# Performance work log

Measured on AMD Instinct MI355X. Metric: run time of the kernel, lower is better.

Reference implementation:

```python
import jax, jax.numpy as jnp
import numpy as np

N_NODES = 50000
N_EDGES = 800000
D_FEAT = 64
UNITS = 64


def setup_inputs() -> dict:
    key = jax.random.key(0)
    k1, k2, k3, k4, k5 = jax.random.split(key, 5)
    embeddings = jax.random.normal(k1, (N_NODES, D_FEAT), dtype=jnp.float32)
    edge_src = jax.random.randint(k2, (N_EDGES,), 0, N_NODES, dtype=jnp.int32)
    edge_dst = jax.random.randint(k3, (N_EDGES,), 0, N_NODES, dtype=jnp.int32)
    # normalized-adjacency-like positive weights
    edge_w = jax.random.uniform(k4, (N_EDGES,), dtype=jnp.float32)
    # keras 'truncated_normal' initializer default stddev=0.05 (approx w/ normal)
    kernel = jax.random.normal(k5, (D_FEAT, UNITS), dtype=jnp.float32) * 0.05
    return {"embeddings": embeddings, "edge_src": edge_src,
            "edge_dst": edge_dst, "edge_w": edge_w, "kernel": kernel}


def reference(embeddings, edge_src, edge_dst, edge_w, kernel):
    # SpMM: agg[i] = sum_{e: dst(e)=i} w_e * embeddings[src(e)]
    msgs = embeddings[edge_src] * edge_w[:, None]            # [E, D]
    agg = jax.ops.segment_sum(msgs, edge_dst,
                              num_segments=embeddings.shape[0])  # [N, D]
    # dense GEMM + relu (use_bias=False)
    return jax.nn.relu(agg @ kernel)                          # [N, units]
```

## Files before the change

kernel.cpp:

```cpp
#include <hip/hip_runtime.h>
#include <hip/hip_bf16.h>

#define D       64
#define CH      4096
#define BKT     32
#define PASS    1024
#define NCOL    16
#define COLMASK 15
#define SCAP    128
#define SCAPSH  7

__global__ __launch_bounds__(256) void front(
    const float* __restrict__ emb,
    const float* __restrict__ W,
    __hip_bfloat16* __restrict__ Zb,
    const int*   __restrict__ src,
    const int*   __restrict__ dst,
    const float* __restrict__ w,
    int*         __restrict__ gcnt,
    int2*        __restrict__ csr,
    int N, int E, int NB, int NC)
{
    __shared__ int2 rec[CH];
    __shared__ int  lcnt[1568];
    __shared__ int  sh[256];

    const int t = threadIdx.x;

    if ((int)blockIdx.x < NC) {
        const int c     = blockIdx.x;
        const int color = c & COLMASK;
        const int e0    = c * CH;
        const int cnt   = min(CH, E - e0);

        for (int b = t; b < NB; b += 256) lcnt[b] = 0;
        __syncthreads();

        int2 myrec[16]; int mypos[16];
        const int4*   s4p = reinterpret_cast<const int4*>(src + e0);
        const int4*   d4p = reinterpret_cast<const int4*>(dst + e0);
        const float4* w4p = reinterpret_cast<const float4*>(w + e0);
#pragma unroll
        for (int i = 0; i < 4; ++i) {
            int g = i * 256 + t;
            if (g * 4 < cnt) {
                int4   s4 = s4p[g];
                int4   d4 = d4p[g];
                float4 w4 = w4p[g];
                int b0 = d4.x >> 5, b1 = d4.y >> 5, b2 = d4.z >> 5, b3 = d4.w >> 5;
                myrec[4*i+0] = make_int2(s4.x | ((d4.x & 31) << 16) | (b0 << 21), __float_as_int(w4.x));
                myrec[4*i+1] = make_int2(s4.y | ((d4.y & 31) << 16) | (b1 << 21), __float_as_int(w4.y));
                myrec[4*i+2] = make_int2(s4.z | ((d4.z & 31) << 16) | (b2 << 21), __float_as_int(w4.z));
                myrec[4*i+3] = make_int2(s4.w | ((d4.w & 31) << 16) | (b3 << 21), __float_as_int(w4.w));
                mypos[4*i+0] = atomicAdd(&lcnt[b0], 1);
                mypos[4*i+1] = atomicAdd(&lcnt[b1], 1);
                mypos[4*i+2] = atomicAdd(&lcnt[b2], 1);
                mypos[4*i+3] = atomicAdd(&lcnt[b3], 1);
            } else {
#pragma unroll
                for (int k = 0; k < 4; ++k) mypos[4*i+k] = -1;
            }
        }
        __syncthreads();

        int hv[7], ps[7], gbase[7];
        const int hbase = t * 7;
#pragma unroll
        for (int k = 0; k < 7; ++k) {
            int b = hbase + k;
            hv[k] = (b < NB) ? lcnt[b] : 0;
        }
#pragma unroll
        for (int k = 0; k < 7; ++k)
            gbase[k] = (hv[k] > 0)
                ? atomicAdd(&gcnt[color * NB + hbase + k], hv[k]) : 0;

        int s = 0;
#pragma unroll
        for (int k = 0; k < 7; ++k) { ps[k] = s; s += hv[k]; }
        sh[t] = s;
        __syncthreads();
        for (int off = 1; off < 256; off <<= 1) {
            int x = (t >= off) ? sh[t - off] : 0;
            __syncthreads();
            sh[t] += x;
            __syncthreads();
        }
        const int hexcl = sh[t] - s;
        __syncthreads();
#pragma unroll
        for (int k = 0; k < 7; ++k) {
            int b = hbase + k;
            if (b < NB) lcnt[b] = hexcl + ps[k];
        }
        __syncthreads();

#pragma unroll
        for (int k = 0; k < 16; ++k) {
            if (mypos[k] >= 0)
                rec[lcnt[(unsigned)myrec[k].x >> 21] + mypos[k]] = myrec[k];
        }
        __syncthreads();

#pragma unroll
        for (int k = 0; k < 7; ++k) {
            int b = hbase + k;
            if (b < NB)
                lcnt[b] = ((color * NB + b) << SCAPSH) + gbase[k] - (hexcl + ps[k]);
        }
        __syncthreads();

        for (int j = t; j < cnt; j += 256) {
            int2 rj = rec[j];
            csr[j + lcnt[(unsigned)rj.x >> 21]] = rj;
        }
        return;
    }

    float* At = (float*)rec;
    const int row0 = ((int)blockIdx.x - NC) * 64;
    const int lane = t & 63;
    const int wave = t >> 6;

    float wcol[D];
#pragma unroll
    for (int k = 0; k < D; ++k) wcol[k] = W[k * D + lane];

    for (int i = t; i < 1024; i += 256) {
        int r = i >> 4, gr = row0 + r;
        float4 v = (gr < N)
            ? reinterpret_cast<const float4*>(emb)[(size_t)gr * 16 + (i & 15)]
            : float4{0.f, 0.f, 0.f, 0.f};
        reinterpret_cast<float4*>(At)[i] = v;
    }
    __syncthreads();

    for (int rr = 0; rr < 16; ++rr) {
        int r = wave * 16 + rr, gr = row0 + r;
        if (gr >= N) break;
        const float4* arow = reinterpret_cast<const float4*>(At + r * D);
        float acc = 0.f;
#pragma unroll
        for (int k4 = 0; k4 < 16; ++k4) {
            float4 a = arow[k4];
            acc = fmaf(a.x, wcol[4 * k4 + 0], acc);
            acc = fmaf(a.y, wcol[4 * k4 + 1], acc);
            acc = fmaf(a.z, wcol[4 * k4 + 2], acc);
            acc = fmaf(a.w, wcol[4 * k4 + 3], acc);
        }
        Zb[(size_t)gr * D + lane] = __float2bfloat16(acc);
    }
}

__global__ __launch_bounds__(256) void aggregate(
    const __hip_bfloat16* __restrict__ Zb,
    const int2* __restrict__ csr,
    const int*  __restrict__ gcnt,
    float*      __restrict__ out,
    int N, int NB)
{
    __shared__ int2 srec[PASS];
    __shared__ int  hist[BKT];
    __shared__ int  nbase[BKT + 1];
    __shared__ int  cpre[NCOL + 1];

    const int t = threadIdx.x;
    const int b = blockIdx.x;

    if (t == 0) {
        int s = 0;
#pragma unroll
        for (int k = 0; k < NCOL; ++k) { cpre[k] = s; s += gcnt[k * NB + b]; }
        cpre[NCOL] = s;
    }
    __syncthreads();
    const int T = cpre[NCOL];

    const int wv = t >> 6, lane = t & 63, slot = lane >> 3, q = lane & 7;
    const int4* Zq = reinterpret_cast<const int4*>(Zb);

    float4 alo[8], ahi[8];
#pragma unroll
    for (int r = 0; r < 8; ++r) { alo[r] = float4{0,0,0,0}; ahi[r] = float4{0,0,0,0}; }

#define FMA8(LO, HI, WW, ZZ)                                                     \
    do {                                                                         \
        (LO).x = fmaf((WW), __uint_as_float((unsigned)(ZZ).x << 16),        (LO).x); \
        (LO).y = fmaf((WW), __uint_as_float((unsigned)(ZZ).x & 0xFFFF0000u),(LO).y); \
        (LO).z = fmaf((WW), __uint_as_float((unsigned)(ZZ).y << 16),        (LO).z); \
        (LO).w = fmaf((WW), __uint_as_float((unsigned)(ZZ).y & 0xFFFF0000u),(LO).w); \
        (HI).x = fmaf((WW), __uint_as_float((unsigned)(ZZ).z << 16),        (HI).x); \
        (HI).y = fmaf((WW), __uint_as_float((unsigned)(ZZ).z & 0xFFFF0000u),(HI).y); \
        (HI).z = fmaf((WW), __uint_as_float((unsigned)(ZZ).w << 16),        (HI).z); \
        (HI).w = fmaf((WW), __uint_as_float((unsigned)(ZZ).w & 0xFFFF0000u),(HI).w); \
    } while (0)

    for (int cur = 0; cur < T; cur += PASS) {
        const int cnt = min(PASS, T - cur);
        if (t < BKT) hist[t] = 0;
        __syncthreads();

        int2 myrec[4]; int mypos[4];
#pragma unroll
        for (int k = 0; k < 4; ++k) {
            int j = k * 256 + t;
            if (j < cnt) {
                int vj = cur + j;
                int kk = 0;
#pragma unroll
                for (int m = 1; m < NCOL; ++m) kk += (vj >= cpre[m]);
                int2 r2 = csr[((kk * NB + b) << SCAPSH) + (vj - cpre[kk])];
                myrec[k] = r2;
                mypos[k] = atomicAdd(&hist[(r2.x >> 16) & (BKT - 1)], 1);
            } else mypos[k] = -1;
        }
        __syncthreads();

        if (t < BKT) {
            int v = hist[t], x = v;
            for (int off = 1; off < BKT; off <<= 1) {
                int y = __shfl_up(x, off, 64);
                if (t >= off) x += y;
            }
            nbase[t] = x - v;
            if (t == BKT - 1) nbase[BKT] = x;
        }
        __syncthreads();

#pragma unroll
        for (int k = 0; k < 4; ++k) {
            if (mypos[k] >= 0)
                srec[nbase[(myrec[k].x >> 16) & (BKT - 1)] + mypos[k]] = myrec[k];
        }
        __syncthreads();

        for (int r = 0; r < 8; ++r) {
            const int nl = wv * 8 + r;
            const int jb = nbase[nl] + slot;
            const int je = nbase[nl + 1];
            const int j1 = jb + 8, j2 = jb + 16;
            int2 e0 = make_int2(0, 0), e1 = make_int2(0, 0), e2 = make_int2(0, 0);
            if (jb < je) e0 = srec[jb];
            if (j1 < je) e1 = srec[j1];
            if (j2 < je) e2 = srec[j2];
            int4 z0 = make_int4(0,0,0,0), z1 = make_int4(0,0,0,0), z2 = make_int4(0,0,0,0);
            if (jb < je) z0 = Zq[(size_t)(e0.x & 0xFFFF) * 8 + q];
            if (j1 < je) z1 = Zq[(size_t)(e1.x & 0xFFFF) * 8 + q];
            if (j2 < je) z2 = Zq[(size_t)(e2.x & 0xFFFF) * 8 + q];
            FMA8(alo[r], ahi[r], __int_as_float(e0.y), z0);
            FMA8(alo[r], ahi[r], __int_as_float(e1.y), z1);
            FMA8(alo[r], ahi[r], __int_as_float(e2.y), z2);
            for (int j = j2 + 8; j < je; j += 8) {
                int2 e = srec[j];
                int4 zz = Zq[(size_t)(e.x & 0xFFFF) * 8 + q];
                FMA8(alo[r], ahi[r], __int_as_float(e.y), zz);
            }
        }
        __syncthreads();
    }

    const int node0 = b * BKT + wv * 8;
#pragma unroll
    for (int r = 0; r < 8; ++r) {
        float4 lo = alo[r], hi = ahi[r];
#pragma unroll
        for (int off = 32; off >= 8; off >>= 1) {
            lo.x += __shfl_down(lo.x, off, 64);
            lo.y += __shfl_down(lo.y, off, 64);
            lo.z += __shfl_down(lo.z, off, 64);
            lo.w += __shfl_down(lo.w, off, 64);
            hi.x += __shfl_down(hi.x, off, 64);
            hi.y += __shfl_down(hi.y, off, 64);
            hi.z += __shfl_down(hi.z, off, 64);
            hi.w += __shfl_down(hi.w, off, 64);
        }
        int node = node0 + r;
        if (lane < 8 && node < N) {
            float4 o0, o1;
            o0.x = fmaxf(lo.x, 0.f); o0.y = fmaxf(lo.y, 0.f);
            o0.z = fmaxf(lo.z, 0.f); o0.w = fmaxf(lo.w, 0.f);
            o1.x = fmaxf(hi.x, 0.f); o1.y = fmaxf(hi.y, 0.f);
            o1.z = fmaxf(hi.z, 0.f); o1.w = fmaxf(hi.w, 0.f);
            float4* orow = reinterpret_cast<float4*>(out) + (size_t)node * 16 + lane * 2;
            orow[0] = o0;
            orow[1] = o1;
        }
    }
#undef FMA8
}

extern "C" void kernel_launch(void* const* d_in, const int* in_sizes, int n_in,
                              void* d_out, int out_size, void* d_ws, size_t ws_size,
                              hipStream_t stream)
{
    const float* emb  = (const float*)d_in[0];
    const int*   esrc = (const int*)  d_in[1];
    const int*   edst = (const int*)  d_in[2];
    const float* ew   = (const float*)d_in[3];
    const float* W    = (const float*)d_in[4];
    float*       out  = (float*)d_out;

    const int N = in_sizes[0] / D;
    const int E = in_sizes[1];

    const int NB        = (N + BKT - 1) / BKT;
    const int NC        = (E + CH - 1) / CH;
    const int gemmTiles = (N + 63) / 64;

    char* p = (char*)d_ws;
    __hip_bfloat16* Zb = (__hip_bfloat16*)p;  p += (size_t)N * D * 2;
    int*  gcnt = (int*)p;                     p += (size_t)NCOL * ((NB + 3) & ~3) * 4;
    int2* csr  = (int2*)p;

    hipMemsetAsync(gcnt, 0, (size_t)NCOL * NB * sizeof(int), stream);

    front<<<NC + gemmTiles, 256, 0, stream>>>(
        emb, W, Zb, esrc, edst, ew, gcnt, csr, N, E, NB, NC);

    aggregate<<<NB, 256, 0, stream>>>(
        Zb, csr, gcnt, out, N, NB);
}
```

Measured before the change: 127.6 us.

## Interleave two nodes' gathers, make GEMM blocks persistent, parallelize color prefix

```diff
diff --git a/kernel.cpp b/kernel.cpp
--- a/kernel.cpp
+++ b/kernel.cpp
@@ -19,7 +19,7 @@
     const float* __restrict__ w,
     int*         __restrict__ gcnt,
     int2*        __restrict__ csr,
-    int N, int E, int NB, int NC)
+    int N, int E, int NB, int NC, int gemmTiles, int gemmBlocks)
 {
     __shared__ int2 rec[CH];
     __shared__ int  lcnt[1568];
@@ -118,7 +118,6 @@
     }
 
     float* At = (float*)rec;
-    const int row0 = ((int)blockIdx.x - NC) * 64;
     const int lane = t & 63;
     const int wave = t >> 6;
 
@@ -126,29 +125,34 @@
 #pragma unroll
     for (int k = 0; k < D; ++k) wcol[k] = W[k * D + lane];
 
-    for (int i = t; i < 1024; i += 256) {
-        int r = i >> 4, gr = row0 + r;
-        float4 v = (gr < N)
-            ? reinterpret_cast<const float4*>(emb)[(size_t)gr * 16 + (i & 15)]
-            : float4{0.f, 0.f, 0.f, 0.f};
-        reinterpret_cast<float4*>(At)[i] = v;
-    }
-    __syncthreads();
-
-    for (int rr = 0; rr < 16; ++rr) {
-        int r = wave * 16 + rr, gr = row0 + r;
-        if (gr >= N) break;
-        const float4* arow = reinterpret_cast<const float4*>(At + r * D);
-        float acc = 0.f;
-#pragma unroll
-        for (int k4 = 0; k4 < 16; ++k4) {
-            float4 a = arow[k4];
-            acc = fmaf(a.x, wcol[4 * k4 + 0], acc);
-            acc = fmaf(a.y, wcol[4 * k4 + 1], acc);
-            acc = fmaf(a.z, wcol[4 * k4 + 2], acc);
-            acc = fmaf(a.w, wcol[4 * k4 + 3], acc);
-        }
-        Zb[(size_t)gr * D + lane] = __float2bfloat16(acc);
+    for (int tile = (int)blockIdx.x - NC; tile < gemmTiles; tile += gemmBlocks) {
+        const int row0 = tile * 64;
+
+        for (int i = t; i < 1024; i += 256) {
+            int r = i >> 4, gr = row0 + r;
+            float4 v = (gr < N)
+                ? reinterpret_cast<const float4*>(emb)[(size_t)gr * 16 + (i & 15)]
+                : float4{0.f, 0.f, 0.f, 0.f};
+            reinterpret_cast<float4*>(At)[i] = v;
+        }
+        __syncthreads();
+
+        for (int rr = 0; rr < 16; ++rr) {
+            int r = wave * 16 + rr, gr = row0 + r;
+            if (gr >= N) break;
+            const float4* arow = reinterpret_cast<const float4*>(At + r * D);
+            float acc = 0.f;
+#pragma unroll
+            for (int k4 = 0; k4 < 16; ++k4) {
+                float4 a = arow[k4];
+                acc = fmaf(a.x, wcol[4 * k4 + 0], acc);
+                acc = fmaf(a.y, wcol[4 * k4 + 1], acc);
+                acc = fmaf(a.z, wcol[4 * k4 + 2], acc);
+                acc = fmaf(a.w, wcol[4 * k4 + 3], acc);
+            }
+            Zb[(size_t)gr * D + lane] = __float2bfloat16(acc);
+        }
+        __syncthreads();
     }
 }
 
@@ -167,21 +171,22 @@
     const int t = threadIdx.x;
     const int b = blockIdx.x;
 
-    if (t == 0) {
-        int s = 0;
-#pragma unroll
-        for (int k = 0; k < NCOL; ++k) { cpre[k] = s; s += gcnt[k * NB + b]; }
-        cpre[NCOL] = s;
+    if (t < NCOL) {
+        int v = gcnt[t * NB + b];
+        int x = v;
+#pragma unroll
+        for (int off = 1; off < NCOL; off <<= 1) {
+            int y = __shfl_up(x, off, 64);
+            if (t >= off) x += y;
+        }
+        cpre[t] = x - v;
+        if (t == NCOL - 1) cpre[NCOL] = x;
     }
     __syncthreads();
     const int T = cpre[NCOL];
 
     const int wv = t >> 6, lane = t & 63, slot = lane >> 3, q = lane & 7;
     const int4* Zq = reinterpret_cast<const int4*>(Zb);
-
-    float4 alo[8], ahi[8];
-#pragma unroll
-    for (int r = 0; r < 8; ++r) { alo[r] = float4{0,0,0,0}; ahi[r] = float4{0,0,0,0}; }
 
 #define FMA8(LO, HI, WW, ZZ)                                                     \
     do {                                                                         \
@@ -195,6 +200,10 @@
         (HI).w = fmaf((WW), __uint_as_float((unsigned)(ZZ).w & 0xFFFF0000u),(HI).w); \
     } while (0)
 
+    float4 accLo[8], accHi[8];
+#pragma unroll
+    for (int r = 0; r < 8; ++r) { accLo[r] = float4{0,0,0,0}; accHi[r] = float4{0,0,0,0}; }
+
     for (int cur = 0; cur < T; cur += PASS) {
         const int cnt = min(PASS, T - cur);
         if (t < BKT) hist[t] = 0;
@@ -234,26 +243,47 @@
         }
         __syncthreads();
 
-        for (int r = 0; r < 8; ++r) {
-            const int nl = wv * 8 + r;
-            const int jb = nbase[nl] + slot;
-            const int je = nbase[nl + 1];
-            const int j1 = jb + 8, j2 = jb + 16;
-            int2 e0 = make_int2(0, 0), e1 = make_int2(0, 0), e2 = make_int2(0, 0);
-            if (jb < je) e0 = srec[jb];
-            if (j1 < je) e1 = srec[j1];
-            if (j2 < je) e2 = srec[j2];
-            int4 z0 = make_int4(0,0,0,0), z1 = make_int4(0,0,0,0), z2 = make_int4(0,0,0,0);
-            if (jb < je) z0 = Zq[(size_t)(e0.x & 0xFFFF) * 8 + q];
-            if (j1 < je) z1 = Zq[(size_t)(e1.x & 0xFFFF) * 8 + q];
-            if (j2 < je) z2 = Zq[(size_t)(e2.x & 0xFFFF) * 8 + q];
-            FMA8(alo[r], ahi[r], __int_as_float(e0.y), z0);
-            FMA8(alo[r], ahi[r], __int_as_float(e1.y), z1);
-            FMA8(alo[r], ahi[r], __int_as_float(e2.y), z2);
-            for (int j = j2 + 8; j < je; j += 8) {
+        for (int rp = 0; rp < 8; rp += 2) {
+            const int nlA = wv * 8 + rp;
+            const int nlB = nlA + 1;
+            const int jbA = nbase[nlA] + slot, jeA = nbase[nlA + 1];
+            const int jbB = nbase[nlB] + slot, jeB = nbase[nlB + 1];
+            const int a1 = jbA + 8, a2 = jbA + 16;
+            const int b1 = jbB + 8, b2 = jbB + 16;
+
+            int2 eA0{0,0}, eA1{0,0}, eA2{0,0}, eB0{0,0}, eB1{0,0}, eB2{0,0};
+            if (jbA < jeA) eA0 = srec[jbA];
+            if (a1  < jeA) eA1 = srec[a1];
+            if (a2  < jeA) eA2 = srec[a2];
+            if (jbB < jeB) eB0 = srec[jbB];
+            if (b1  < jeB) eB1 = srec[b1];
+            if (b2  < jeB) eB2 = srec[b2];
+
+            int4 zA0{0,0,0,0}, zA1{0,0,0,0}, zA2{0,0,0,0};
+            int4 zB0{0,0,0,0}, zB1{0,0,0,0}, zB2{0,0,0,0};
+            if (jbA < jeA) zA0 = Zq[(size_t)(eA0.x & 0xFFFF) * 8 + q];
+            if (jbB < jeB) zB0 = Zq[(size_t)(eB0.x & 0xFFFF) * 8 + q];
+            if (a1  < jeA) zA1 = Zq[(size_t)(eA1.x & 0xFFFF) * 8 + q];
+            if (b1  < jeB) zB1 = Zq[(size_t)(eB1.x & 0xFFFF) * 8 + q];
+            if (a2  < jeA) zA2 = Zq[(size_t)(eA2.x & 0xFFFF) * 8 + q];
+            if (b2  < jeB) zB2 = Zq[(size_t)(eB2.x & 0xFFFF) * 8 + q];
+
+            FMA8(accLo[rp],   accHi[rp],   __int_as_float(eA0.y), zA0);
+            FMA8(accLo[rp+1], accHi[rp+1], __int_as_float(eB0.y), zB0);
+            FMA8(accLo[rp],   accHi[rp],   __int_as_float(eA1.y), zA1);
+            FMA8(accLo[rp+1], accHi[rp+1], __int_as_float(eB1.y), zB1);
+            FMA8(accLo[rp],   accHi[rp],   __int_as_float(eA2.y), zA2);
+            FMA8(accLo[rp+1], accHi[rp+1], __int_as_float(eB2.y), zB2);
+
+            for (int j = a2 + 8; j < jeA; j += 8) {
                 int2 e = srec[j];
                 int4 zz = Zq[(size_t)(e.x & 0xFFFF) * 8 + q];
-                FMA8(alo[r], ahi[r], __int_as_float(e.y), zz);
+                FMA8(accLo[rp], accHi[rp], __int_as_float(e.y), zz);
+            }
+            for (int j = b2 + 8; j < jeB; j += 8) {
+                int2 e = srec[j];
+                int4 zz = Zq[(size_t)(e.x & 0xFFFF) * 8 + q];
+                FMA8(accLo[rp+1], accHi[rp+1], __int_as_float(e.y), zz);
             }
         }
         __syncthreads();
@@ -262,7 +292,7 @@
     const int node0 = b * BKT + wv * 8;
 #pragma unroll
     for (int r = 0; r < 8; ++r) {
-        float4 lo = alo[r], hi = ahi[r];
+        float4 lo = accLo[r], hi = accHi[r];
 #pragma unroll
         for (int off = 32; off >= 8; off >>= 1) {
             lo.x += __shfl_down(lo.x, off, 64);
@@ -303,9 +333,10 @@
     const int N = in_sizes[0] / D;
     const int E = in_sizes[1];
 
-    const int NB        = (N + BKT - 1) / BKT;
-    const int NC        = (E + CH - 1) / CH;
-    const int gemmTiles = (N + 63) / 64;
+    const int NB         = (N + BKT - 1) / BKT;
+    const int NC         = (E + CH - 1) / CH;
+    const int gemmTiles  = (N + 63) / 64;
+    const int gemmBlocks = (gemmTiles + 1) / 2;
 
     char* p = (char*)d_ws;
     __hip_bfloat16* Zb = (__hip_bfloat16*)p;  p += (size_t)N * D * 2;
@@ -314,8 +345,8 @@
 
     hipMemsetAsync(gcnt, 0, (size_t)NCOL * NB * sizeof(int), stream);
 
-    front<<<NC + gemmTiles, 256, 0, stream>>>(
-        emb, W, Zb, esrc, edst, ew, gcnt, csr, N, E, NB, NC);
+    front<<<NC + gemmBlocks, 256, 0, stream>>>(
+        emb, W, Zb, esrc, edst, ew, gcnt, csr, N, E, NB, NC, gemmTiles, gemmBlocks);
 
     aggregate<<<NB, 256, 0, stream>>>(
         Zb, csr, gcnt, out, N, NB);
```

After: 131.8 us. 1.03x slower.
